# Performance work log

Measured on AMD Instinct MI355X. Metric: run time of the kernel, lower is better.

## Reference

```python
import jax, jax.numpy as jnp
import numpy as np

IN_FEATURES = 4096
OUT_FEATURES = 11008
BATCH, SEQ = 8, 16


def setup_inputs() -> dict:
    key = jax.random.key(0)
    k_in, k_w, k_s, k_b = jax.random.split(key, 4)
    inp = jax.random.normal(k_in, (BATCH, SEQ, IN_FEATURES), dtype=jnp.float32)
    # int8 weights in [-128, 127], as torch.randint(-128, 127, ...)
    quantized_weights = jax.random.randint(
        k_w, (OUT_FEATURES, IN_FEATURES), -128, 127, dtype=jnp.int32
    ).astype(jnp.int8)
    scales = jax.random.normal(k_s, (OUT_FEATURES,), dtype=jnp.float32)
    bias = jax.random.normal(k_b, (1, OUT_FEATURES), dtype=jnp.float32)
    return {"input": inp, "quantized_weights": quantized_weights,
            "scales": scales, "bias": bias}


def reference(input, quantized_weights, scales, bias):
    # dequantize weight to activation dtype, then linear: y = x @ W^T
    w = quantized_weights.astype(input.dtype)  # [O, I]
    out = jnp.einsum("bsi,oi->bso", input, w)  # [B, S, O]
    out = out * scales  # per-output-channel scale
    out = out + bias    # bias shape [1, O] broadcasts
    return out
```

## Files before the change

### kernel.cpp

```cpp
#include <hip/hip_runtime.h>
#include <stdint.h>


#define M_ROWS 128
#define K_DIM  4096
#define N_DIM  11008
#define CHUNKS 64
#define NT64   (N_DIM / 64)
#define KSPLIT 4
#define CPB    (CHUNKS / KSPLIT)
#define XP_BYTES (M_ROWS * K_DIM * 2)
#define PART_ELEMS ((size_t)M_ROWS * (size_t)N_DIM)

typedef __attribute__((ext_vector_type(8))) short bf16x8;
typedef __attribute__((ext_vector_type(4))) float f32x4;
typedef const unsigned __attribute__((address_space(1)))* gas1_t;
typedef unsigned __attribute__((address_space(3)))* las3_t;

__device__ __forceinline__ unsigned bf16_rn(float f) {
  unsigned u = __float_as_uint(f);
  return (u + 0x7FFFu + ((u >> 16) & 1u)) >> 16;
}
__device__ __forceinline__ unsigned pk2(int a, int b) {
  unsigned lo = __float_as_uint((float)a), hi = __float_as_uint((float)b);
#if __has_builtin(__builtin_amdgcn_perm)
  return __builtin_amdgcn_perm(hi, lo, 0x07060302u);
#else
  return (hi & 0xFFFF0000u) | (lo >> 16);
#endif
}

__device__ __forceinline__ void gload_lds16(const void* g, void* lds) {
#if __has_builtin(__builtin_amdgcn_global_load_lds)
  __builtin_amdgcn_global_load_lds((gas1_t)g, (las3_t)(size_t)(unsigned)(size_t)lds,
                                   16, 0, 0);
#else
  *(uint4*)lds = *(const uint4*)g;
#endif
}

#define BAR()    asm volatile("s_barrier" ::: "memory")
#define WBAR16() asm volatile("s_waitcnt vmcnt(16)\n\ts_barrier" ::: "memory")
#define WBAR8()  asm volatile("s_waitcnt vmcnt(8)\n\ts_barrier" ::: "memory")
#define WBAR0()  asm volatile("s_waitcnt vmcnt(0)\n\ts_barrier" ::: "memory")

__global__ __launch_bounds__(256) void pack_x_kernel(
    const float* __restrict__ x, unsigned short* __restrict__ xp) {
  int tid  = blockIdx.x * 256 + threadIdx.x;
  int lane = tid & 63;
  int h    = (tid >> 6) & 1;
  int mf   = (tid >> 7) & 7;
  int kk   = tid >> 10;
  int m     = mf * 16 + (lane & 15);
  int kbase = kk * 64 + h * 32 + ((lane >> 4) * 8);
  const float* src = x + (size_t)m * K_DIM + kbase;
  float4 f0 = *(const float4*)(src);
  float4 f1 = *(const float4*)(src + 4);
  float v[8] = {f0.x, f0.y, f0.z, f0.w, f1.x, f1.y, f1.z, f1.w};
  unsigned po[4];
#pragma unroll
  for (int i = 0; i < 4; ++i)
    po[i] = bf16_rn(v[2 * i]) | (bf16_rn(v[2 * i + 1]) << 16);
  *(uint4*)(xp + (size_t)tid * 8) = *(uint4*)po;
}

struct BReg { uint4 v[4]; };

__global__ __launch_bounds__(256, 3) void gemm4w_kernel(
    const unsigned short* __restrict__ xp,
    const int* __restrict__ wq,
    float* __restrict__ part) {
  __shared__ char As[3 * 16384];

  const int tid  = threadIdx.x;
  const int lane = tid & 63;
  const int w    = tid >> 6;
  const int nt   = blockIdx.x;
  const int kz   = blockIdx.y;
  const int kk0  = kz * CPB;
  const size_t n0 = (size_t)nt * 64 + (size_t)w * 16;
  const int l15 = lane & 15, lh = lane >> 4;

  const char* agp = (const char*)xp + (size_t)kk0 * 16384 + tid * 16;
  const int* bptr = wq + (n0 + (size_t)l15) * K_DIM + (size_t)kk0 * 64 + lh * 8;

  f32x4 acc[8];
  {
    f32x4 z = {0.f, 0.f, 0.f, 0.f};
#pragma unroll
    for (int i = 0; i < 8; ++i) acc[i] = z;
  }

  auto STAGE = [&](int t, int bufOff) {
#pragma unroll
    for (int i = 0; i < 4; ++i)
      gload_lds16(agp + (size_t)t * 16384 + (size_t)i * 4096,
                  As + bufOff + tid * 16 + i * 4096);
  };
  auto LOADB = [&](int t, BReg& R) {
    const int* bp = bptr + t * 64;
    R.v[0] = *(const uint4*)(bp);
    R.v[1] = *(const uint4*)(bp + 4);
    R.v[2] = *(const uint4*)(bp + 32);
    R.v[3] = *(const uint4*)(bp + 36);
  };
  auto COMP = [&](const char* ab, BReg& R) {
    bf16x8 cv[2];
#pragma unroll
    for (int s = 0; s < 2; ++s) {
      union { unsigned u[4]; bf16x8 b; } c;
      c.u[0] = pk2((int)R.v[s * 2].x,     (int)R.v[s * 2].y);
      c.u[1] = pk2((int)R.v[s * 2].z,     (int)R.v[s * 2].w);
      c.u[2] = pk2((int)R.v[s * 2 + 1].x, (int)R.v[s * 2 + 1].y);
      c.u[3] = pk2((int)R.v[s * 2 + 1].z, (int)R.v[s * 2 + 1].w);
      cv[s] = c.b;
    }
#pragma unroll
    for (int mf = 0; mf < 8; ++mf)
#pragma unroll
      for (int s = 0; s < 2; ++s) {
        bf16x8 a = *(const bf16x8*)(ab + (mf * 2 + s) * 1024 + lane * 16);
        acc[mf] = __builtin_amdgcn_mfma_f32_16x16x32_bf16(a, cv[s], acc[mf], 0, 0, 0);
      }
  };

#define PHASE(T, CBUF, NBUF, RC, RN)              \
    LOADB((T) + 2, RN);                           \
    BAR();                                        \
    STAGE((T) + 2, (NBUF) * 16384);               \
    WBAR16();                                     \
    COMP(As + (CBUF) * 16384, RC);

  BReg R0, R1, R2;
  STAGE(0, 0);
  LOADB(0, R0);
  STAGE(1, 16384);
  LOADB(1, R1);

#pragma unroll 1
  for (int t = 0; t < 12; t += 3) {
    PHASE(t + 0, 0, 2, R0, R2);
    PHASE(t + 1, 1, 0, R1, R0);
    PHASE(t + 2, 2, 1, R2, R1);
  }
  PHASE(12, 0, 2, R0, R2);
  PHASE(13, 1, 0, R1, R0);
  WBAR8();
  COMP(As + 2 * 16384, R2);
  WBAR0();
  COMP(As + 0 * 16384, R0);
#undef PHASE

  float* pb = part + (size_t)kz * PART_ELEMS + n0 + l15;
#pragma unroll
  for (int mf = 0; mf < 8; ++mf) {
    const int mb = mf * 16 + lh * 4;
#pragma unroll
    for (int r = 0; r < 4; ++r)
      pb[(size_t)(mb + r) * N_DIM] = acc[mf][r];
  }
}

__global__ __launch_bounds__(256) void reduce_kernel(
    const float* __restrict__ part, const float* __restrict__ scales,
    const float* __restrict__ bias, float* __restrict__ out) {
  const int m = blockIdx.y;
  const int c4 = blockIdx.x * 256 + threadIdx.x;
  if (c4 >= N_DIM / 4) return;
  const size_t n = (size_t)c4 * 4;
  const float* p = part + (size_t)m * N_DIM + n;
  float4 s = *(const float4*)(p);
#pragma unroll
  for (int z = 1; z < KSPLIT; ++z) {
    float4 q = *(const float4*)(p + (size_t)z * PART_ELEMS);
    s.x += q.x; s.y += q.y; s.z += q.z; s.w += q.w;
  }
  float4 sc = *(const float4*)(scales + n);
  float4 bi = *(const float4*)(bias + n);
  float4 r;
  r.x = sc.x * s.x + bi.x;
  r.y = sc.y * s.y + bi.y;
  r.z = sc.z * s.z + bi.z;
  r.w = sc.w * s.w + bi.w;
  *(float4*)(out + (size_t)m * N_DIM + n) = r;
}

__global__ __launch_bounds__(256) void naive_kernel(
    const float* __restrict__ x, const int* __restrict__ wq,
    const float* __restrict__ scales, const float* __restrict__ bias,
    float* __restrict__ out) {
  const int n = blockIdx.x * 256 + threadIdx.x;
  const int m = blockIdx.y;
  const float* xr = x + (size_t)m * K_DIM;
  const int* wr = wq + (size_t)n * K_DIM;
  float s = 0.f;
  for (int k = 0; k < K_DIM; k += 4) {
    float4 xv = *(const float4*)(xr + k);
    int4  wv = *(const int4*)(wr + k);
    s += xv.x * (float)wv.x + xv.y * (float)wv.y +
         xv.z * (float)wv.z + xv.w * (float)wv.w;
  }
  out[(size_t)m * N_DIM + n] = scales[n] * s + bias[n];
}

extern "C" void kernel_launch(void* const* d_in, const int* in_sizes, int n_in,
                              void* d_out, int out_size, void* d_ws, size_t ws_size,
                              hipStream_t stream) {
  const float* x      = (const float*)d_in[0];
  const int* wq       = (const int*)d_in[1];
  const float* scales = (const float*)d_in[2];
  const float* bias   = (const float*)d_in[3];
  float* out          = (float*)d_out;

  const size_t need = (size_t)XP_BYTES + KSPLIT * PART_ELEMS * sizeof(float);
  if (ws_size < need) {
    naive_kernel<<<dim3(N_DIM / 256, M_ROWS), 256, 0, stream>>>(x, wq, scales, bias, out);
    return;
  }
  unsigned short* xp = (unsigned short*)d_ws;
  float* part        = (float*)((char*)d_ws + XP_BYTES);

  pack_x_kernel<<<256, 256, 0, stream>>>(x, xp);
  gemm4w_kernel<<<dim3(NT64, KSPLIT), 256, 0, stream>>>(xp, wq, part);
  reduce_kernel<<<dim3((N_DIM / 4 + 255) / 256, M_ROWS), 256, 0, stream>>>(
      part, scales, bias, out);
}
```

Before: 52.55 us.

## Replace split-K partial buffers and reduce kernel with scaled atomic adds

```diff
diff --git a/kernel.cpp b/kernel.cpp
--- a/kernel.cpp
+++ b/kernel.cpp
@@ -7,10 +7,9 @@
 #define N_DIM  11008
 #define CHUNKS 64
 #define NT64   (N_DIM / 64)
-#define KSPLIT 4
+#define KSPLIT 8
 #define CPB    (CHUNKS / KSPLIT)
 #define XP_BYTES (M_ROWS * K_DIM * 2)
-#define PART_ELEMS ((size_t)M_ROWS * (size_t)N_DIM)
 
 typedef __attribute__((ext_vector_type(8))) short bf16x8;
 typedef __attribute__((ext_vector_type(4))) float f32x4;
@@ -43,6 +42,15 @@
 #define WBAR16() asm volatile("s_waitcnt vmcnt(16)\n\ts_barrier" ::: "memory")
 #define WBAR8()  asm volatile("s_waitcnt vmcnt(8)\n\ts_barrier" ::: "memory")
 #define WBAR0()  asm volatile("s_waitcnt vmcnt(0)\n\ts_barrier" ::: "memory")
+
+__global__ __launch_bounds__(256) void init_out_kernel(
+    const float* __restrict__ bias, float* __restrict__ out) {
+  const int idx = blockIdx.x * 256 + threadIdx.x;
+  const int n4 = N_DIM / 4;
+  if (idx >= M_ROWS * n4) return;
+  const int c = idx % n4;
+  ((float4*)out)[idx] = ((const float4*)bias)[c];
+}
 
 __global__ __launch_bounds__(256) void pack_x_kernel(
     const float* __restrict__ x, unsigned short* __restrict__ xp) {
@@ -69,7 +77,8 @@
 __global__ __launch_bounds__(256, 3) void gemm4w_kernel(
     const unsigned short* __restrict__ xp,
     const int* __restrict__ wq,
-    float* __restrict__ part) {
+    const float* __restrict__ scales,
+    float* __restrict__ out) {
   __shared__ char As[3 * 16384];
 
   const int tid  = threadIdx.x;
@@ -138,51 +147,27 @@
   LOADB(1, R1);
 
 #pragma unroll 1
-  for (int t = 0; t < 12; t += 3) {
+  for (int t = 0; t < 6; t += 3) {
     PHASE(t + 0, 0, 2, R0, R2);
     PHASE(t + 1, 1, 0, R1, R0);
     PHASE(t + 2, 2, 1, R2, R1);
   }
-  PHASE(12, 0, 2, R0, R2);
-  PHASE(13, 1, 0, R1, R0);
   WBAR8();
-  COMP(As + 2 * 16384, R2);
+  COMP(As + 0 * 16384, R0);
   WBAR0();
-  COMP(As + 0 * 16384, R0);
+  COMP(As + 1 * 16384, R1);
 #undef PHASE
 
-  float* pb = part + (size_t)kz * PART_ELEMS + n0 + l15;
+  const size_t n = n0 + (size_t)l15;
+  const float sc = scales[n];
+  float* ob = out + n;
 #pragma unroll
   for (int mf = 0; mf < 8; ++mf) {
     const int mb = mf * 16 + lh * 4;
 #pragma unroll
     for (int r = 0; r < 4; ++r)
-      pb[(size_t)(mb + r) * N_DIM] = acc[mf][r];
-  }
-}
-
-__global__ __launch_bounds__(256) void reduce_kernel(
-    const float* __restrict__ part, const float* __restrict__ scales,
-    const float* __restrict__ bias, float* __restrict__ out) {
-  const int m = blockIdx.y;
-  const int c4 = blockIdx.x * 256 + threadIdx.x;
-  if (c4 >= N_DIM / 4) return;
-  const size_t n = (size_t)c4 * 4;
-  const float* p = part + (size_t)m * N_DIM + n;
-  float4 s = *(const float4*)(p);
-#pragma unroll
-  for (int z = 1; z < KSPLIT; ++z) {
-    float4 q = *(const float4*)(p + (size_t)z * PART_ELEMS);
-    s.x += q.x; s.y += q.y; s.z += q.z; s.w += q.w;
-  }
-  float4 sc = *(const float4*)(scales + n);
-  float4 bi = *(const float4*)(bias + n);
-  float4 r;
-  r.x = sc.x * s.x + bi.x;
-  r.y = sc.y * s.y + bi.y;
-  r.z = sc.z * s.z + bi.z;
-  r.w = sc.w * s.w + bi.w;
-  *(float4*)(out + (size_t)m * N_DIM + n) = r;
+      atomicAdd(ob + (size_t)(mb + r) * N_DIM, sc * acc[mf][r]);
+  }
 }
 
 __global__ __launch_bounds__(256) void naive_kernel(
@@ -212,16 +197,13 @@
   const float* bias   = (const float*)d_in[3];
   float* out          = (float*)d_out;
 
-  const size_t need = (size_t)XP_BYTES + KSPLIT * PART_ELEMS * sizeof(float);
-  if (ws_size < need) {
+  if (ws_size < (size_t)XP_BYTES) {
     naive_kernel<<<dim3(N_DIM / 256, M_ROWS), 256, 0, stream>>>(x, wq, scales, bias, out);
     return;
   }
   unsigned short* xp = (unsigned short*)d_ws;
-  float* part        = (float*)((char*)d_ws + XP_BYTES);
-
+
+  init_out_kernel<<<dim3((M_ROWS * N_DIM / 4 + 255) / 256), 256, 0, stream>>>(bias, out);
   pack_x_kernel<<<256, 256, 0, stream>>>(x, xp);
-  gemm4w_kernel<<<dim3(NT64, KSPLIT), 256, 0, stream>>>(xp, wq, part);
-  reduce_kernel<<<dim3((N_DIM / 4 + 255) / 256, M_ROWS), 256, 0, stream>>>(
-      part, scales, bias, out);
-}
+  gemm4w_kernel<<<dim3(NT64, KSPLIT), 256, 0, stream>>>(xp, wq, scales, out);
+}
```

After: 65.37 us. 1.24x slower.
